# Kernel optimization log

Hardware: AMD Instinct MI355X
Metric: run time of the kernel (lower is better)

The kernel has to match this reference:

```python
import jax, jax.numpy as jnp
import numpy as np

NEG_INF = -1e30

def setup_inputs() -> dict:
    key = jax.random.key(0)
    ks = jax.random.split(key, 7)
    B, S, D = 2, 4096, 128
    scale = 1.0 / np.sqrt(D)
    return {
        "x": jax.random.normal(ks[0], (B, S, D), jnp.float32),
        "Wq": jax.random.normal(ks[1], (D, D), jnp.float32) * scale,
        "bq": jax.random.normal(ks[2], (D,), jnp.float32) * 0.01,
        "Wk": jax.random.normal(ks[3], (D, D), jnp.float32) * scale,
        "bk": jax.random.normal(ks[4], (D,), jnp.float32) * 0.01,
        "Wv": jax.random.normal(ks[5], (D, D), jnp.float32) * scale,
        "bv": jax.random.normal(ks[6], (D,), jnp.float32) * 0.01,
        "window_size": 128,
    }

def reference(x, Wq, bq, Wk, bk, Wv, bv, window_size):
    B, S, D = x.shape
    half = window_size // 2
    q = x @ Wq + bq
    k = x @ Wk + bk
    v = x @ Wv + bv
    # banded window indices: for query i, keys in [i-half, i+half]
    offs = jnp.arange(-half, half + 1)          # [W] with W = 2*half+1
    idx = jnp.arange(S)[:, None] + offs[None, :]  # [S, W]
    valid = (idx >= 0) & (idx < S)
    idxc = jnp.clip(idx, 0, S - 1)
    kw = k[:, idxc, :]  # [B, S, W, D]
    vw = v[:, idxc, :]  # [B, S, W, D]
    scores = jnp.einsum('bsd,bswd->bsw', q, kw) / jnp.sqrt(jnp.float32(D))
    scores = jnp.where(valid[None], scores, NEG_INF)
    attn = jax.nn.softmax(scores, axis=-1)
    out = jnp.einsum('bsw,bswd->bsd', attn, vw)
    return out
```

## Files before the change

### kernel.cpp

```cpp
#include <hip/hip_runtime.h>
#include <hip/hip_bf16.h>

typedef __attribute__((ext_vector_type(8))) short short8;
typedef __attribute__((ext_vector_type(4))) float f32x4;

union U16x8 { uint4 u; short8 s; unsigned short us[8]; };

#define S_LEN 4096
#define DH    128
#define TQ    32
#define KW    160
#define KSTR  136
#define VSTR  138
#define PSTR  168

__global__ __launch_bounds__(256) void qkv_kernel(
    const float* __restrict__ x,
    const float* __restrict__ Wq, const float* __restrict__ bq,
    const float* __restrict__ Wk, const float* __restrict__ bk,
    const float* __restrict__ Wv, const float* __restrict__ bv,
    __hip_bfloat16* __restrict__ q, __hip_bfloat16* __restrict__ k,
    __hip_bfloat16* __restrict__ v)
{
    const int t = threadIdx.x;
    const int j = t & 127;
    const int g = t >> 7;
    const int row0 = blockIdx.x * 16;

    __shared__ float xs[16][DH];
    for (int c = t; c < 512; c += 256) {
        int r = c >> 5, f = c & 31;
        ((float4*)xs[r])[f] = ((const float4*)(x + (size_t)(row0 + r) * DH))[f];
    }
    __syncthreads();

    float aq[8], ak[8], av[8];
    const float bqv = bq[j], bkv = bk[j], bvv = bv[j];
    #pragma unroll
    for (int r = 0; r < 8; ++r) { aq[r] = bqv; ak[r] = bkv; av[r] = bvv; }

    #pragma unroll 2
    for (int d4 = 0; d4 < 32; ++d4) {
        float4 xv[8];
        #pragma unroll
        for (int r = 0; r < 8; ++r) xv[r] = *(const float4*)&xs[g*8 + r][d4*4];
        #pragma unroll
        for (int dd = 0; dd < 4; ++dd) {
            int d = d4*4 + dd;
            float wq = Wq[d*DH + j], wk = Wk[d*DH + j], wv = Wv[d*DH + j];
            #pragma unroll
            for (int r = 0; r < 8; ++r) {
                float xvs = (&xv[r].x)[dd];
                aq[r] = fmaf(xvs, wq, aq[r]);
                ak[r] = fmaf(xvs, wk, ak[r]);
                av[r] = fmaf(xvs, wv, av[r]);
            }
        }
    }
    #pragma unroll
    for (int r = 0; r < 8; ++r) {
        size_t o = (size_t)(row0 + g*8 + r) * DH + j;
        q[o] = __float2bfloat16(aq[r]);
        k[o] = __float2bfloat16(ak[r]);
        v[o] = __float2bfloat16(av[r]);
    }
}

__global__ __launch_bounds__(256) void attn_kernel(
    const __hip_bfloat16* __restrict__ qg,
    const __hip_bfloat16* __restrict__ kg,
    const __hip_bfloat16* __restrict__ vg,
    float* __restrict__ out, const int* __restrict__ wsz)
{
    __shared__ __align__(16) unsigned short KV[KW * VSTR];
    __shared__ __align__(16) __hip_bfloat16 Ps[2][16 * PSTR];
    __shared__ float pmax[2][2][16];
    __shared__ float psum[2][2][16];

    const int t    = threadIdx.x;
    const int qblk = blockIdx.x;
    const int b    = qblk >> 7;
    const int s0   = (qblk & 127) * TQ;
    const int k0   = s0 - 64;
    const int half = wsz[0] >> 1;

    const int wave = t >> 6, lane = t & 63;
    const int rb = wave >> 1, cc = wave & 1;
    const int i = lane & 15, g = lane >> 4;

    const __hip_bfloat16* kbase = kg + (size_t)b * S_LEN * DH;
    const __hip_bfloat16* vbase = vg + (size_t)b * S_LEN * DH;

    for (int c = t; c < KW * 16; c += 256) {
        int row = c >> 4, cg = c & 15;
        int key = k0 + row;
        uint4 val = make_uint4(0u, 0u, 0u, 0u);
        if (key >= 0 && key < S_LEN)
            val = *(const uint4*)(kbase + (size_t)key * DH + cg*8);
        *(uint4*)&KV[row * KSTR + cg*8] = val;
    }

    short8 aq[4];
    {
        const __hip_bfloat16* qrow = qg + (size_t)(b * S_LEN + s0 + rb*16 + i) * DH;
        #pragma unroll
        for (int kc = 0; kc < 4; ++kc) {
            U16x8 u; u.u = *(const uint4*)(qrow + kc*32 + g*8);
            aq[kc] = u.s;
        }
    }
    __syncthreads();

    f32x4 acc[5];
    #pragma unroll
    for (int kt = 0; kt < 5; ++kt) { acc[kt][0]=0.f; acc[kt][1]=0.f; acc[kt][2]=0.f; acc[kt][3]=0.f; }
    #pragma unroll
    for (int kt = 0; kt < 5; ++kt) {
        int col0 = cc*80 + kt*16;
        #pragma unroll
        for (int kc = 0; kc < 4; ++kc) {
            short8 bk = *(short8*)&KV[(col0 + i) * KSTR + kc*32 + g*8];
            acc[kt] = __builtin_amdgcn_mfma_f32_16x16x32_bf16(aq[kc], bk, acc[kt], 0, 0, 0);
        }
    }

    const float scale = 0.08838834764831845f;
    float sc[5][4], m4[4];
    #pragma unroll
    for (int r = 0; r < 4; ++r) m4[r] = -3e30f;
    #pragma unroll
    for (int kt = 0; kt < 5; ++kt) {
        int key = k0 + cc*80 + kt*16 + i;
        #pragma unroll
        for (int r = 0; r < 4; ++r) {
            int qrow = s0 + rb*16 + g*4 + r;
            bool valid = (key >= 0) && (key < S_LEN) && (key >= qrow - half) && (key <= qrow + half);
            float sv = valid ? acc[kt][r] * scale : -1e30f;
            sc[kt][r] = sv;
            m4[r] = fmaxf(m4[r], sv);
        }
    }
    #pragma unroll
    for (int r = 0; r < 4; ++r) {
        #pragma unroll
        for (int m = 1; m < 16; m <<= 1)
            m4[r] = fmaxf(m4[r], __shfl_xor(m4[r], m, 64));
    }
    if (i == 0) {
        #pragma unroll
        for (int r = 0; r < 4; ++r) pmax[rb][cc][g*4 + r] = m4[r];
    }
    __syncthreads();

    uint4 vstage[10];
    #pragma unroll
    for (int idx = 0; idx < 10; ++idx) {
        int c = t + idx*256;
        int row = c >> 4, cg = c & 15;
        int key = k0 + row;
        uint4 val = make_uint4(0u, 0u, 0u, 0u);
        if (key >= 0 && key < S_LEN)
            val = *(const uint4*)(vbase + (size_t)key * DH + cg*8);
        vstage[idx] = val;
    }

    float M[4], l4[4];
    #pragma unroll
    for (int r = 0; r < 4; ++r) {
        M[r] = fmaxf(m4[r], pmax[rb][cc ^ 1][g*4 + r]);
        l4[r] = 0.f;
    }
    #pragma unroll
    for (int kt = 0; kt < 5; ++kt) {
        #pragma unroll
        for (int r = 0; r < 4; ++r) {
            float p = __expf(sc[kt][r] - M[r]);
            l4[r] += p;
            Ps[rb][(g*4 + r) * PSTR + cc*80 + kt*16 + i] = __float2bfloat16(p);
        }
    }
    #pragma unroll
    for (int r = 0; r < 4; ++r) {
        #pragma unroll
        for (int m = 1; m < 16; m <<= 1)
            l4[r] += __shfl_xor(l4[r], m, 64);
    }
    if (i == 0) {
        #pragma unroll
        for (int r = 0; r < 4; ++r) psum[rb][cc][g*4 + r] = l4[r];
    }

    #pragma unroll
    for (int idx = 0; idx < 10; ++idx) {
        int c = t + idx*256;
        int row = c >> 4, cg = c & 15;
        unsigned int* dst = (unsigned int*)((char*)KV + (size_t)(row * VSTR + cg*8) * 2);
        dst[0] = vstage[idx].x; dst[1] = vstage[idx].y;
        dst[2] = vstage[idx].z; dst[3] = vstage[idx].w;
    }
    __syncthreads();

    float linv[4];
    #pragma unroll
    for (int r = 0; r < 4; ++r)
        linv[r] = 1.0f / (psum[rb][0][g*4 + r] + psum[rb][1][g*4 + r]);

    short8 ap[5];
    #pragma unroll
    for (int kc = 0; kc < 5; ++kc)
        ap[kc] = *(short8*)&Ps[rb][i * PSTR + kc*32 + g*8];

    f32x4 oacc[4];
    #pragma unroll
    for (int nt = 0; nt < 4; ++nt) { oacc[nt][0]=0.f; oacc[nt][1]=0.f; oacc[nt][2]=0.f; oacc[nt][3]=0.f; }

    const unsigned short* Vu = KV;
    #pragma unroll
    for (int nt = 0; nt < 4; ++nt) {
        int n0 = cc*64 + nt*16;
        #pragma unroll
        for (int kc = 0; kc < 5; ++kc) {
            U16x8 bu;
            #pragma unroll
            for (int jj = 0; jj < 8; ++jj)
                bu.us[jj] = Vu[(kc*32 + g*8 + jj) * VSTR + n0 + i];
            oacc[nt] = __builtin_amdgcn_mfma_f32_16x16x32_bf16(ap[kc], bu.s, oacc[nt], 0, 0, 0);
        }
    }

    #pragma unroll
    for (int nt = 0; nt < 4; ++nt) {
        #pragma unroll
        for (int r = 0; r < 4; ++r) {
            int qrow = s0 + rb*16 + g*4 + r;
            out[((size_t)(b * S_LEN) + qrow) * DH + cc*64 + nt*16 + i] = oacc[nt][r] * linv[r];
        }
    }
}

extern "C" void kernel_launch(void* const* d_in, const int* in_sizes, int n_in,
                              void* d_out, int out_size, void* d_ws, size_t ws_size,
                              hipStream_t stream) {
    const float* x  = (const float*)d_in[0];
    const float* Wq = (const float*)d_in[1];
    const float* bq = (const float*)d_in[2];
    const float* Wk = (const float*)d_in[3];
    const float* bk = (const float*)d_in[4];
    const float* Wv = (const float*)d_in[5];
    const float* bv = (const float*)d_in[6];
    const int* wsz  = (const int*)d_in[7];

    const int B = 2, S = 4096;
    const int N = B * S;

    __hip_bfloat16* q = (__hip_bfloat16*)d_ws;
    __hip_bfloat16* k = q + (size_t)N * DH;
    __hip_bfloat16* v = k + (size_t)N * DH;

    qkv_kernel<<<N / 16, 256, 0, stream>>>(x, Wq, bq, Wk, bk, Wv, bv, q, k, v);
    attn_kernel<<<N / TQ, 256, 0, stream>>>(q, k, v, (float*)d_out, wsz);
}
```

Baseline: 100.4 us.

## Shrink query tile, read K from global, and store V transposed with swizzle

Each attention block now handles 16 queries instead of 32, which doubles the grid, and splits the 10 key tiles across 4 waves. K fragments are loaded straight from global memory into MFMA operands instead of being staged in shared memory. V is loaded early into registers, transposed with byte-permute ops and written to shared memory in a swizzled transposed layout, so the PV MFMA can read it with 16-byte vector loads instead of eight scalar 2-byte reads. The cost is that K/V halo rows are reloaded more often across the smaller tiles, and register pressure rises from holding V in registers.

```diff
diff --git a/kernel.cpp b/kernel.cpp
--- a/kernel.cpp
+++ b/kernel.cpp
@@ -8,11 +8,10 @@
 
 #define S_LEN 4096
 #define DH    128
-#define TQ    32
-#define KW    160
-#define KSTR  136
-#define VSTR  138
-#define PSTR  168
+#define TQ    16
+#define KEYS  160
+#define VTS   168
+#define PST   168
 
 __global__ __launch_bounds__(256) void qkv_kernel(
     const float* __restrict__ x,
@@ -66,78 +65,123 @@
     }
 }
 
+__device__ inline void vt_xpose_write(unsigned short* VT, const uint4* vr,
+                                      int kgp, int dgp)
+{
+    unsigned w[8][4];
+    #pragma unroll
+    for (int p = 0; p < 4; ++p) {
+        #pragma unroll
+        for (int j = 0; j < 4; ++j) {
+            unsigned xlo = ((const unsigned*)&vr[2*p])[j];
+            unsigned ylo = ((const unsigned*)&vr[2*p+1])[j];
+            w[2*j][p]   = __builtin_amdgcn_perm(ylo, xlo, 0x05040100u);
+            w[2*j+1][p] = __builtin_amdgcn_perm(ylo, xlo, 0x07060302u);
+        }
+    }
+    int sw = kgp + (dgp & 7); if (sw >= 21) sw -= 21;
+    #pragma unroll
+    for (int d = 0; d < 8; ++d) {
+        int row = dgp*8 + d;
+        *(uint4*)&VT[row*VTS + sw*8] =
+            make_uint4(w[d][0], w[d][1], w[d][2], w[d][3]);
+    }
+}
+
 __global__ __launch_bounds__(256) void attn_kernel(
     const __hip_bfloat16* __restrict__ qg,
     const __hip_bfloat16* __restrict__ kg,
     const __hip_bfloat16* __restrict__ vg,
     float* __restrict__ out, const int* __restrict__ wsz)
 {
-    __shared__ __align__(16) unsigned short KV[KW * VSTR];
-    __shared__ __align__(16) __hip_bfloat16 Ps[2][16 * PSTR];
-    __shared__ float pmax[2][2][16];
-    __shared__ float psum[2][2][16];
+    __shared__ __align__(16) unsigned short VT[128 * VTS];
+    __shared__ __align__(16) unsigned short Pm[TQ * PST];
+    __shared__ float pmax[4][16];
+    __shared__ float psum[4][16];
 
     const int t    = threadIdx.x;
+    const int wave = t >> 6, lane = t & 63;
+    const int i = lane & 15, g = lane >> 4;
     const int qblk = blockIdx.x;
-    const int b    = qblk >> 7;
-    const int s0   = (qblk & 127) * TQ;
+    const int b    = qblk >> 8;
+    const int s0   = (qblk & 255) * TQ;
     const int k0   = s0 - 64;
     const int half = wsz[0] >> 1;
-
-    const int wave = t >> 6, lane = t & 63;
-    const int rb = wave >> 1, cc = wave & 1;
-    const int i = lane & 15, g = lane >> 4;
-
-    const __hip_bfloat16* kbase = kg + (size_t)b * S_LEN * DH;
-    const __hip_bfloat16* vbase = vg + (size_t)b * S_LEN * DH;
-
-    for (int c = t; c < KW * 16; c += 256) {
-        int row = c >> 4, cg = c & 15;
-        int key = k0 + row;
-        uint4 val = make_uint4(0u, 0u, 0u, 0u);
+    const float scale = 0.08838834764831845f;
+
+    const __hip_bfloat16* kb = kg + (size_t)b * S_LEN * DH;
+    const __hip_bfloat16* vb = vg + (size_t)b * S_LEN * DH;
+
+    const int kgp0 = t >> 4, dgp0 = t & 15;
+    const bool two = (t & 3) == 0;
+    const int tau2 = 256 + (t >> 2);
+    const int kgp1 = tau2 >> 4, dgp1 = tau2 & 15;
+    uint4 vr0[8], vr1[8];
+    #pragma unroll
+    for (int r = 0; r < 8; ++r) {
+        int key = k0 + kgp0*8 + r;
+        uint4 val = make_uint4(0u,0u,0u,0u);
         if (key >= 0 && key < S_LEN)
-            val = *(const uint4*)(kbase + (size_t)key * DH + cg*8);
-        *(uint4*)&KV[row * KSTR + cg*8] = val;
+            val = *(const uint4*)(vb + (size_t)key * DH + dgp0*8);
+        vr0[r] = val;
+    }
+    #pragma unroll
+    for (int r = 0; r < 8; ++r) {
+        int key = k0 + kgp1*8 + r;
+        uint4 val = make_uint4(0u,0u,0u,0u);
+        if (two && key >= 0 && key < S_LEN)
+            val = *(const uint4*)(vb + (size_t)key * DH + dgp1*8);
+        vr1[r] = val;
     }
 
     short8 aq[4];
     {
-        const __hip_bfloat16* qrow = qg + (size_t)(b * S_LEN + s0 + rb*16 + i) * DH;
+        const __hip_bfloat16* qrow = qg + (size_t)(b * S_LEN + s0 + i) * DH;
         #pragma unroll
         for (int kc = 0; kc < 4; ++kc) {
             U16x8 u; u.u = *(const uint4*)(qrow + kc*32 + g*8);
             aq[kc] = u.s;
         }
     }
-    __syncthreads();
-
-    f32x4 acc[5];
-    #pragma unroll
-    for (int kt = 0; kt < 5; ++kt) { acc[kt][0]=0.f; acc[kt][1]=0.f; acc[kt][2]=0.f; acc[kt][3]=0.f; }
-    #pragma unroll
-    for (int kt = 0; kt < 5; ++kt) {
-        int col0 = cc*80 + kt*16;
-        #pragma unroll
-        for (int kc = 0; kc < 4; ++kc) {
-            short8 bk = *(short8*)&KV[(col0 + i) * KSTR + kc*32 + g*8];
-            acc[kt] = __builtin_amdgcn_mfma_f32_16x16x32_bf16(aq[kc], bk, acc[kt], 0, 0, 0);
-        }
-    }
-
-    const float scale = 0.08838834764831845f;
-    float sc[5][4], m4[4];
+
+    const int nkt = (wave < 2) ? 3 : 2;
+    f32x4 acc[3];
+    #pragma unroll
+    for (int u = 0; u < 3; ++u) { acc[u][0]=0.f; acc[u][1]=0.f; acc[u][2]=0.f; acc[u][3]=0.f; }
+    #pragma unroll
+    for (int u = 0; u < 3; ++u) {
+        if (u < nkt) {
+            int kt = wave + 4*u;
+            int key = k0 + kt*16 + i;
+            const __hip_bfloat16* krow = kb + (ptrdiff_t)key * DH;
+            #pragma unroll
+            for (int kc = 0; kc < 4; ++kc) {
+                U16x8 u16v; u16v.u = *(const uint4*)(krow + kc*32 + g*8);
+                acc[u] = __builtin_amdgcn_mfma_f32_16x16x32_bf16(aq[kc], u16v.s, acc[u], 0, 0, 0);
+            }
+        }
+    }
+
+    vt_xpose_write(VT, vr0, kgp0, dgp0);
+    if (two) vt_xpose_write(VT, vr1, kgp1, dgp1);
+
+    float sc[3][4], m4[4];
     #pragma unroll
     for (int r = 0; r < 4; ++r) m4[r] = -3e30f;
     #pragma unroll
-    for (int kt = 0; kt < 5; ++kt) {
-        int key = k0 + cc*80 + kt*16 + i;
-        #pragma unroll
-        for (int r = 0; r < 4; ++r) {
-            int qrow = s0 + rb*16 + g*4 + r;
-            bool valid = (key >= 0) && (key < S_LEN) && (key >= qrow - half) && (key <= qrow + half);
-            float sv = valid ? acc[kt][r] * scale : -1e30f;
-            sc[kt][r] = sv;
-            m4[r] = fmaxf(m4[r], sv);
+    for (int u = 0; u < 3; ++u) {
+        if (u < nkt) {
+            int kt = wave + 4*u;
+            int key = k0 + kt*16 + i;
+            #pragma unroll
+            for (int r = 0; r < 4; ++r) {
+                int qrow = s0 + g*4 + r;
+                bool valid = (key >= 0) && (key < S_LEN) &&
+                             (key >= qrow - half) && (key <= qrow + half);
+                float sv = valid ? acc[u][r] * scale : -1e30f;
+                sc[u][r] = sv;
+                m4[r] = fmaxf(m4[r], sv);
+            }
         }
     }
     #pragma unroll
@@ -148,35 +192,28 @@
     }
     if (i == 0) {
         #pragma unroll
-        for (int r = 0; r < 4; ++r) pmax[rb][cc][g*4 + r] = m4[r];
+        for (int r = 0; r < 4; ++r) pmax[wave][g*4 + r] = m4[r];
     }
     __syncthreads();
 
-    uint4 vstage[10];
-    #pragma unroll
-    for (int idx = 0; idx < 10; ++idx) {
-        int c = t + idx*256;
-        int row = c >> 4, cg = c & 15;
-        int key = k0 + row;
-        uint4 val = make_uint4(0u, 0u, 0u, 0u);
-        if (key >= 0 && key < S_LEN)
-            val = *(const uint4*)(vbase + (size_t)key * DH + cg*8);
-        vstage[idx] = val;
-    }
-
     float M[4], l4[4];
     #pragma unroll
     for (int r = 0; r < 4; ++r) {
-        M[r] = fmaxf(m4[r], pmax[rb][cc ^ 1][g*4 + r]);
+        int qr = g*4 + r;
+        M[r] = fmaxf(fmaxf(pmax[0][qr], pmax[1][qr]), fmaxf(pmax[2][qr], pmax[3][qr]));
         l4[r] = 0.f;
     }
     #pragma unroll
-    for (int kt = 0; kt < 5; ++kt) {
-        #pragma unroll
-        for (int r = 0; r < 4; ++r) {
-            float p = __expf(sc[kt][r] - M[r]);
-            l4[r] += p;
-            Ps[rb][(g*4 + r) * PSTR + cc*80 + kt*16 + i] = __float2bfloat16(p);
+    for (int u = 0; u < 3; ++u) {
+        if (u < nkt) {
+            int kt = wave + 4*u;
+            #pragma unroll
+            for (int r = 0; r < 4; ++r) {
+                float p = __expf(sc[u][r] - M[r]);
+                l4[r] += p;
+                __hip_bfloat16 pb = __float2bfloat16(p);
+                Pm[(g*4 + r) * PST + kt*16 + i] = *(unsigned short*)&pb;
+            }
         }
     }
     #pragma unroll
@@ -187,53 +224,45 @@
     }
     if (i == 0) {
         #pragma unroll
-        for (int r = 0; r < 4; ++r) psum[rb][cc][g*4 + r] = l4[r];
-    }
-
-    #pragma unroll
-    for (int idx = 0; idx < 10; ++idx) {
-        int c = t + idx*256;
-        int row = c >> 4, cg = c & 15;
-        unsigned int* dst = (unsigned int*)((char*)KV + (size_t)(row * VSTR + cg*8) * 2);
-        dst[0] = vstage[idx].x; dst[1] = vstage[idx].y;
-        dst[2] = vstage[idx].z; dst[3] = vstage[idx].w;
+        for (int r = 0; r < 4; ++r) psum[wave][g*4 + r] = l4[r];
     }
     __syncthreads();
 
     float linv[4];
     #pragma unroll
-    for (int r = 0; r < 4; ++r)
-        linv[r] = 1.0f / (psum[rb][0][g*4 + r] + psum[rb][1][g*4 + r]);
+    for (int r = 0; r < 4; ++r) {
+        int qr = g*4 + r;
+        linv[r] = 1.0f / (psum[0][qr] + psum[1][qr] + psum[2][qr] + psum[3][qr]);
+    }
 
     short8 ap[5];
     #pragma unroll
     for (int kc = 0; kc < 5; ++kc)
-        ap[kc] = *(short8*)&Ps[rb][i * PSTR + kc*32 + g*8];
-
-    f32x4 oacc[4];
-    #pragma unroll
-    for (int nt = 0; nt < 4; ++nt) { oacc[nt][0]=0.f; oacc[nt][1]=0.f; oacc[nt][2]=0.f; oacc[nt][3]=0.f; }
-
-    const unsigned short* Vu = KV;
-    #pragma unroll
-    for (int nt = 0; nt < 4; ++nt) {
-        int n0 = cc*64 + nt*16;
+        ap[kc] = *(const short8*)&Pm[i * PST + kc*32 + g*8];
+
+    const int n0 = wave * 32;
+    f32x4 oacc[2];
+    #pragma unroll
+    for (int nt = 0; nt < 2; ++nt) { oacc[nt][0]=0.f; oacc[nt][1]=0.f; oacc[nt][2]=0.f; oacc[nt][3]=0.f; }
+    #pragma unroll
+    for (int nt = 0; nt < 2; ++nt) {
+        int row0 = n0 + nt*16 + i;
+        int dgr = (row0 >> 3) & 7;
         #pragma unroll
         for (int kc = 0; kc < 5; ++kc) {
-            U16x8 bu;
-            #pragma unroll
-            for (int jj = 0; jj < 8; ++jj)
-                bu.us[jj] = Vu[(kc*32 + g*8 + jj) * VSTR + n0 + i];
-            oacc[nt] = __builtin_amdgcn_mfma_f32_16x16x32_bf16(ap[kc], bu.s, oacc[nt], 0, 0, 0);
-        }
-    }
-
-    #pragma unroll
-    for (int nt = 0; nt < 4; ++nt) {
+            int lg = 4*kc + g;
+            int sw = lg + dgr; if (sw >= 21) sw -= 21;
+            short8 bv = *(const short8*)&VT[row0 * VTS + sw*8];
+            oacc[nt] = __builtin_amdgcn_mfma_f32_16x16x32_bf16(ap[kc], bv, oacc[nt], 0, 0, 0);
+        }
+    }
+
+    #pragma unroll
+    for (int nt = 0; nt < 2; ++nt) {
         #pragma unroll
         for (int r = 0; r < 4; ++r) {
-            int qrow = s0 + rb*16 + g*4 + r;
-            out[((size_t)(b * S_LEN) + qrow) * DH + cc*64 + nt*16 + i] = oacc[nt][r] * linv[r];
+            int qrow = s0 + g*4 + r;
+            out[((size_t)(b * S_LEN) + qrow) * DH + n0 + nt*16 + i] = oacc[nt][r] * linv[r];
         }
     }
 }
```

Result: no change. 99.84 us (-0.6%).
